# Kernel tuning notes

Hardware: AMD Instinct MI355X
Metric: run time of the kernel (lower is better)

## Reference

```python
import jax, jax.numpy as jnp
import numpy as np

M = 4096        # reference column size (init kwarg m)
TAU = 1.0       # temperature
SLICE_LEN = 4096


def setup_inputs() -> dict:
    key = jax.random.key(0)
    scores = jax.random.normal(key, (4, 131072), dtype=jnp.float32)
    return {"scores": scores}


def reference(scores):
    B, n = scores.shape
    m = min(M, n)
    # global top-m (sorted descending, matching torch.topk sorted=True)
    ref_val, ref_idx = jax.lax.top_k(scores, m)          # (B, m), (B, m)

    n_chunks = n // SLICE_LEN
    # (n_chunks, B, SLICE_LEN): scan over token chunks so only one
    # (B, SLICE_LEN, m) pairwise block is live at a time, as in the torch loop.
    chunks = jnp.swapaxes(scores.reshape(B, n_chunks, SLICE_LEN), 0, 1)

    def step(_, slice_scores):
        # pairwise = -|s_i - ref_j| / tau  -> softmax over m -> argmax -> gather
        pairwise = -jnp.abs(slice_scores[..., None] - ref_val[:, None, :]) / TAU
        P_hat = jax.nn.softmax(pairwise, axis=-1)        # (B, SLICE_LEN, m)
        col_rank = jnp.argmax(P_hat, axis=-1)            # (B, SLICE_LEN)
        perm_slice = jnp.take_along_axis(ref_idx, col_rank, axis=1)
        return None, perm_slice

    _, perms = jax.lax.scan(step, None, chunks)          # (n_chunks, B, SLICE_LEN)
    perm = jnp.swapaxes(perms, 0, 1).reshape(B, n)       # (B, n) int32 indices
    return perm
```

## Files before the change

### kernel.cpp

```cpp
#include <hip/hip_runtime.h>
#include <stdint.h>

#define BROWS 4
#define NCOLS 131072
#define MREF  4096
#define HIST_BITS 13
#define NBUCK (1 << HIST_BITS)
#define USHIFT (32 - HIST_BITS)
#define CAP 6144
#define HIST_BLK_PER_ROW 8
#define NPART 32
#define PQUOTA 192
#define PARTCAP 1024

__device__ __forceinline__ uint32_t orderable(float f) {
    uint32_t u = __float_as_uint(f);
    return (u & 0x80000000u) ? ~u : (u | 0x80000000u);
}
__device__ __forceinline__ float unorderable(uint32_t u) {
    uint32_t b = (u & 0x80000000u) ? (u & 0x7FFFFFFFu) : ~u;
    return __uint_as_float(b);
}

__global__ void k_zero(uint32_t* hist) {
    int i = blockIdx.x * blockDim.x + threadIdx.x;
    int tot = BROWS * NBUCK;
    for (; i < tot; i += gridDim.x * blockDim.x) hist[i] = 0u;
}

__global__ void k_hist(const float* __restrict__ sc, uint32_t* __restrict__ hist) {
    __shared__ uint32_t h[NBUCK];
    for (int t = threadIdx.x; t < NBUCK; t += blockDim.x) h[t] = 0u;
    __syncthreads();
    int row  = blockIdx.x / HIST_BLK_PER_ROW;
    int part = blockIdx.x % HIST_BLK_PER_ROW;
    const int CHUNK = NCOLS / HIST_BLK_PER_ROW;
    const float* p = sc + row * NCOLS + part * CHUNK;
    for (int c = threadIdx.x; c < CHUNK; c += blockDim.x) {
        uint32_t u = orderable(p[c]);
        atomicAdd(&h[u >> USHIFT], 1u);
    }
    __syncthreads();
    uint32_t* g = hist + (row << HIST_BITS);
    for (int t = threadIdx.x; t < NBUCK; t += blockDim.x) {
        uint32_t v = h[t];
        if (v) atomicAdd(&g[t], v);
    }
}

__global__ void k_thresh(const uint32_t* __restrict__ hist, uint32_t* __restrict__ Hrow,
                         int* __restrict__ Bs, uint32_t* __restrict__ pcur,
                         uint32_t* __restrict__ pse) {
    __shared__ uint32_t part[256];
    int row = blockIdx.x;
    const uint32_t* h = hist + (row << HIST_BITS);
    int bhi = NBUCK - 1 - (int)threadIdx.x * 32;
    uint32_t run = 0;
    for (int k = 0; k < 32; ++k) run += h[bhi - k];
    part[threadIdx.x] = run;
    __syncthreads();
    if (threadIdx.x == 0) {
        int      Bloc[NPART];
        uint32_t Ploc[NPART];
        for (int p = 0; p < NPART; ++p) { Bloc[p] = -1; Ploc[p] = 0u; }
        uint32_t cum = 0, T = 0;
        int H = 0, pi = 1;
        bool done = false;
        for (int t = 0; t < 256 && !done; ++t) {
            uint32_t cafter = cum + part[t];
            bool cross = (cafter >= (uint32_t)MREF) ||
                         (pi < NPART && cafter >= (uint32_t)(pi * PQUOTA));
            if (cross) {
                int tp = NBUCK - 1 - t * 32;
                for (int k2 = 0; k2 < 32 && !done; ++k2) {
                    int b = tp - k2;
                    uint32_t prev = cum;
                    cum += h[b];
                    while (pi < NPART && cum >= (uint32_t)(pi * PQUOTA)) {
                        Bloc[pi] = b; Ploc[pi] = prev; ++pi;
                    }
                    if (cum >= (uint32_t)MREF) { H = b; T = cum; done = true; }
                }
            } else {
                cum = cafter;
            }
        }
        for (int p = pi; p < NPART; ++p) { Bloc[p] = H - 1; Ploc[p] = T; }
        if (T > (uint32_t)CAP) T = (uint32_t)CAP;
        Hrow[row] = (uint32_t)H;
        Bs[row * NPART + 0] = NBUCK;
        for (int p = 1; p < NPART; ++p) Bs[row * NPART + p] = Bloc[p];
        for (int p = 0; p < NPART; ++p) {
            uint32_t st = Ploc[p];
            if (st > (uint32_t)CAP) st = (uint32_t)CAP;
            pcur[row * NPART + p] = st;
            pse[row * (NPART + 1) + p] = st;
        }
        pse[row * (NPART + 1) + NPART] = T;
    }
}

__global__ void k_compact(const float* __restrict__ sc, const uint32_t* __restrict__ Hrow,
                          const int* __restrict__ Bs, uint32_t* __restrict__ pcur,
                          uint64_t* __restrict__ cand) {
    __shared__ int bsL[NPART];
    __shared__ uint32_t cntP[NPART];
    __shared__ uint32_t baseP[NPART];
    int row = blockIdx.x >> 7;
    int base = (blockIdx.x & 127) << 10;
    uint32_t H = Hrow[row];
    if (threadIdx.x < NPART) {
        bsL[threadIdx.x] = Bs[row * NPART + threadIdx.x];
        cntP[threadIdx.x] = 0u;
    }
    __syncthreads();
    const float* p = sc + row * NCOLS + base;

    uint32_t myu[4], mycol[4], myr[4];
    int myp[4];
    uint32_t n = 0;
    for (int k = 0; k < 4; ++k) {
        int c = (int)threadIdx.x + (k << 8);
        uint32_t u = orderable(p[c]);
        uint32_t b = u >> USHIFT;
        if (b >= H) {
            int pp = 0;
            for (int q = 1; q < NPART; ++q) pp += ((int)b <= bsL[q]) ? 1 : 0;
            myu[n] = u; mycol[n] = (uint32_t)(base + c); myp[n] = pp;
            myr[n] = atomicAdd(&cntP[pp], 1u);
            ++n;
        }
    }
    __syncthreads();
    if (threadIdx.x < NPART)
        baseP[threadIdx.x] = atomicAdd(&pcur[row * NPART + threadIdx.x], cntP[threadIdx.x]);
    __syncthreads();
    uint64_t* cr = cand + (size_t)row * CAP;
    for (uint32_t k = 0; k < n; ++k) {
        uint32_t idx = baseP[myp[k]] + myr[k];
        if (idx < (uint32_t)CAP)
            cr[idx] = ((uint64_t)(~myu[k]) << 32) | mycol[k];
    }
}

__global__ void k_psort(const uint32_t* __restrict__ pse, uint64_t* __restrict__ cand,
                        float* __restrict__ rv, uint32_t* __restrict__ ri) {
    __shared__ uint64_t lds[PARTCAP];
    int row = blockIdx.x >> 5;
    int pp  = blockIdx.x & 31;
    uint32_t start = pse[row * (NPART + 1) + pp];
    uint32_t end   = pse[row * (NPART + 1) + pp + 1];
    if (end > (uint32_t)CAP) end = (uint32_t)CAP;
    uint32_t n = (end > start) ? (end - start) : 0u;
    if (n > (uint32_t)PARTCAP) n = (uint32_t)PARTCAP;
    uint64_t* seg = cand + (size_t)row * CAP + start;
    for (uint32_t i = threadIdx.x; i < (uint32_t)PARTCAP; i += blockDim.x)
        lds[i] = (i < n) ? seg[i] : ~0ULL;
    __syncthreads();
    for (uint32_t k = 2; k <= (uint32_t)PARTCAP; k <<= 1) {
        for (uint32_t j = k >> 1; j > 0; j >>= 1) {
            for (uint32_t i = threadIdx.x; i < (uint32_t)PARTCAP; i += blockDim.x) {
                uint32_t ixj = i ^ j;
                if (ixj > i) {
                    uint64_t a = lds[i], bb = lds[ixj];
                    bool up = ((i & k) == 0);
                    if ((a > bb) == up) { lds[i] = bb; lds[ixj] = a; }
                }
            }
            __syncthreads();
        }
    }
    for (uint32_t i = threadIdx.x; i < n; i += blockDim.x) {
        uint32_t gpos = start + i;
        if (gpos < (uint32_t)MREF) {
            uint64_t key = lds[i];
            uint32_t u = ~(uint32_t)(key >> 32);
            rv[row * MREF + gpos] = unorderable(u);
            ri[row * MREF + gpos] = (uint32_t)(key & 0xFFFFFFFFu);
        }
    }
}

__global__ void k_map(const float* __restrict__ sc, const float* __restrict__ rv,
                      const uint32_t* __restrict__ ri, int* __restrict__ out) {
    __shared__ float srv[MREF];
    int row = blockIdx.x >> 9;
    int col = ((blockIdx.x & 511) << 8) + threadIdx.x;
    const float* rvr = rv + row * MREF;
    for (int t = threadIdx.x; t < MREF; t += blockDim.x) srv[t] = rvr[t];
    __syncthreads();

    float s = sc[row * NCOLS + col];
    int lo = 0, hi = MREF;
    while (lo < hi) { int mid = (lo + hi) >> 1; if (srv[mid] <= s) hi = mid; else lo = mid + 1; }
    int p = lo, jmin;
    if (p == 0) jmin = 0;
    else if (p == MREF) jmin = MREF - 1;
    else {
        float dp = fabsf(s - srv[p]);
        float dm = fabsf(s - srv[p - 1]);
        jmin = (dm <= dp) ? (p - 1) : p;
    }
    float pmax = -fabsf(s - srv[jmin]);
    int jans = jmin;
    for (int j = jmin - 1; j >= 0; --j) {
        float pw = -fabsf(s - srv[j]);
        if (expf(pw - pmax) == 1.0f) jans = j; else break;
    }
    out[row * NCOLS + col] = (int)ri[row * MREF + jans];
}

extern "C" void kernel_launch(void* const* d_in, const int* in_sizes, int n_in,
                              void* d_out, int out_size, void* d_ws, size_t ws_size,
                              hipStream_t stream) {
    const float* sc = (const float*)d_in[0];
    int* out = (int*)d_out;
    char* w = (char*)d_ws;

    uint32_t* hist = (uint32_t*)w;
    uint32_t* Hrow = (uint32_t*)(w + 131072);
    int*      Bs   = (int*)     (w + 131200);
    uint32_t* pcur = (uint32_t*)(w + 131712);
    uint32_t* pse  = (uint32_t*)(w + 132224);
    uint64_t* cand = (uint64_t*)(w + 132864);
    float*    rv   = (float*)   (w + 329472);
    uint32_t* ri   = (uint32_t*)(w + 395008);

    k_zero   <<<64, 256, 0, stream>>>(hist);
    k_hist   <<<BROWS * HIST_BLK_PER_ROW, 256, 0, stream>>>(sc, hist);
    k_thresh <<<BROWS, 256, 0, stream>>>(hist, Hrow, Bs, pcur, pse);
    k_compact<<<512, 256, 0, stream>>>(sc, Hrow, Bs, pcur, cand);
    k_psort  <<<BROWS * NPART, 512, 0, stream>>>(pse, cand, rv, ri);
    k_map    <<<BROWS * 512, 256, 0, stream>>>(sc, rv, ri, out);
}
```

Before: 69.39 us.

## Drop zero and compact kernels; per-block histogram slots and fused partition scan in sort

Each histogram block now writes its private histogram to its own slot, and the threshold kernel sums the slots. This removes the zeroing kernel and the global atomics. The compaction kernel is removed: each partition-sort block scans the whole row and collects elements in its bucket range directly into LDS with a shared-memory atomic counter. This saves two launches and the candidate buffer round trip, but every one of the 128 sort blocks now reads a full 512KB row, so global read traffic grows about 32x for that stage.

Result: slower. 128.7 us (+85.4%).

```diff
diff --git a/kernel.cpp b/kernel.cpp
--- a/kernel.cpp
+++ b/kernel.cpp
@@ -7,7 +7,6 @@
 #define HIST_BITS 13
 #define NBUCK (1 << HIST_BITS)
 #define USHIFT (32 - HIST_BITS)
-#define CAP 6144
 #define HIST_BLK_PER_ROW 8
 #define NPART 32
 #define PQUOTA 192
@@ -22,13 +21,7 @@
     return __uint_as_float(b);
 }
 
-__global__ void k_zero(uint32_t* hist) {
-    int i = blockIdx.x * blockDim.x + threadIdx.x;
-    int tot = BROWS * NBUCK;
-    for (; i < tot; i += gridDim.x * blockDim.x) hist[i] = 0u;
-}
-
-__global__ void k_hist(const float* __restrict__ sc, uint32_t* __restrict__ hist) {
+__global__ void k_hist(const float* __restrict__ sc, uint32_t* __restrict__ hslot) {
     __shared__ uint32_t h[NBUCK];
     for (int t = threadIdx.x; t < NBUCK; t += blockDim.x) h[t] = 0u;
     __syncthreads();
@@ -41,19 +34,22 @@
         atomicAdd(&h[u >> USHIFT], 1u);
     }
     __syncthreads();
-    uint32_t* g = hist + (row << HIST_BITS);
-    for (int t = threadIdx.x; t < NBUCK; t += blockDim.x) {
-        uint32_t v = h[t];
-        if (v) atomicAdd(&g[t], v);
-    }
+    uint32_t* g = hslot + ((size_t)(row * HIST_BLK_PER_ROW + part)) * NBUCK;
+    for (int t = threadIdx.x; t < NBUCK; t += blockDim.x) g[t] = h[t];
 }
 
-__global__ void k_thresh(const uint32_t* __restrict__ hist, uint32_t* __restrict__ Hrow,
-                         int* __restrict__ Bs, uint32_t* __restrict__ pcur,
-                         uint32_t* __restrict__ pse) {
+__global__ void k_thresh(const uint32_t* __restrict__ hslot, uint32_t* __restrict__ Hrow,
+                         int* __restrict__ Bs, uint32_t* __restrict__ pse) {
+    __shared__ uint32_t h[NBUCK];
     __shared__ uint32_t part[256];
     int row = blockIdx.x;
-    const uint32_t* h = hist + (row << HIST_BITS);
+    const uint32_t* basep = hslot + (size_t)row * HIST_BLK_PER_ROW * NBUCK;
+    for (int t = threadIdx.x; t < NBUCK; t += blockDim.x) {
+        uint32_t s = 0;
+        for (int sl = 0; sl < HIST_BLK_PER_ROW; ++sl) s += basep[sl * NBUCK + t];
+        h[t] = s;
+    }
+    __syncthreads();
     int bhi = NBUCK - 1 - (int)threadIdx.x * 32;
     uint32_t run = 0;
     for (int k = 0; k < 32; ++k) run += h[bhi - k];
@@ -86,76 +82,42 @@
             }
         }
         for (int p = pi; p < NPART; ++p) { Bloc[p] = H - 1; Ploc[p] = T; }
-        if (T > (uint32_t)CAP) T = (uint32_t)CAP;
         Hrow[row] = (uint32_t)H;
-        Bs[row * NPART + 0] = NBUCK;
-        for (int p = 1; p < NPART; ++p) Bs[row * NPART + p] = Bloc[p];
-        for (int p = 0; p < NPART; ++p) {
-            uint32_t st = Ploc[p];
-            if (st > (uint32_t)CAP) st = (uint32_t)CAP;
-            pcur[row * NPART + p] = st;
-            pse[row * (NPART + 1) + p] = st;
-        }
+        Bs[row * (NPART + 1) + 0] = NBUCK;
+        for (int p = 1; p < NPART; ++p) Bs[row * (NPART + 1) + p] = Bloc[p];
+        Bs[row * (NPART + 1) + NPART] = H - 1;
+        for (int p = 0; p < NPART; ++p) pse[row * (NPART + 1) + p] = Ploc[p];
         pse[row * (NPART + 1) + NPART] = T;
     }
 }
 
-__global__ void k_compact(const float* __restrict__ sc, const uint32_t* __restrict__ Hrow,
-                          const int* __restrict__ Bs, uint32_t* __restrict__ pcur,
-                          uint64_t* __restrict__ cand) {
-    __shared__ int bsL[NPART];
-    __shared__ uint32_t cntP[NPART];
-    __shared__ uint32_t baseP[NPART];
-    int row = blockIdx.x >> 7;
-    int base = (blockIdx.x & 127) << 10;
-    uint32_t H = Hrow[row];
-    if (threadIdx.x < NPART) {
-        bsL[threadIdx.x] = Bs[row * NPART + threadIdx.x];
-        cntP[threadIdx.x] = 0u;
-    }
+__global__ void k_psort(const float* __restrict__ sc, const int* __restrict__ Bs,
+                        const uint32_t* __restrict__ pse,
+                        float* __restrict__ rv, uint32_t* __restrict__ ri) {
+    __shared__ uint64_t lds[PARTCAP];
+    __shared__ uint32_t cnt;
+    int row = blockIdx.x >> 5;
+    int pp  = blockIdx.x & 31;
+    int hi = Bs[row * (NPART + 1) + pp];
+    int lo = Bs[row * (NPART + 1) + pp + 1];
+    uint32_t start = pse[row * (NPART + 1) + pp];
+    if (threadIdx.x == 0) cnt = 0u;
     __syncthreads();
-    const float* p = sc + row * NCOLS + base;
-
-    uint32_t myu[4], mycol[4], myr[4];
-    int myp[4];
-    uint32_t n = 0;
-    for (int k = 0; k < 4; ++k) {
-        int c = (int)threadIdx.x + (k << 8);
+    const float* p = sc + row * NCOLS;
+    for (int c = (int)threadIdx.x; c < NCOLS; c += (int)blockDim.x) {
         uint32_t u = orderable(p[c]);
-        uint32_t b = u >> USHIFT;
-        if (b >= H) {
-            int pp = 0;
-            for (int q = 1; q < NPART; ++q) pp += ((int)b <= bsL[q]) ? 1 : 0;
-            myu[n] = u; mycol[n] = (uint32_t)(base + c); myp[n] = pp;
-            myr[n] = atomicAdd(&cntP[pp], 1u);
-            ++n;
+        int b = (int)(u >> USHIFT);
+        if (b > lo && b <= hi) {
+            uint32_t pos = atomicAdd(&cnt, 1u);
+            if (pos < (uint32_t)PARTCAP)
+                lds[pos] = ((uint64_t)(~u) << 32) | (uint32_t)c;
         }
     }
     __syncthreads();
-    if (threadIdx.x < NPART)
-        baseP[threadIdx.x] = atomicAdd(&pcur[row * NPART + threadIdx.x], cntP[threadIdx.x]);
-    __syncthreads();
-    uint64_t* cr = cand + (size_t)row * CAP;
-    for (uint32_t k = 0; k < n; ++k) {
-        uint32_t idx = baseP[myp[k]] + myr[k];
-        if (idx < (uint32_t)CAP)
-            cr[idx] = ((uint64_t)(~myu[k]) << 32) | mycol[k];
-    }
-}
-
-__global__ void k_psort(const uint32_t* __restrict__ pse, uint64_t* __restrict__ cand,
-                        float* __restrict__ rv, uint32_t* __restrict__ ri) {
-    __shared__ uint64_t lds[PARTCAP];
-    int row = blockIdx.x >> 5;
-    int pp  = blockIdx.x & 31;
-    uint32_t start = pse[row * (NPART + 1) + pp];
-    uint32_t end   = pse[row * (NPART + 1) + pp + 1];
-    if (end > (uint32_t)CAP) end = (uint32_t)CAP;
-    uint32_t n = (end > start) ? (end - start) : 0u;
+    uint32_t n = cnt;
     if (n > (uint32_t)PARTCAP) n = (uint32_t)PARTCAP;
-    uint64_t* seg = cand + (size_t)row * CAP + start;
-    for (uint32_t i = threadIdx.x; i < (uint32_t)PARTCAP; i += blockDim.x)
-        lds[i] = (i < n) ? seg[i] : ~0ULL;
+    for (uint32_t i = n + threadIdx.x; i < (uint32_t)PARTCAP; i += blockDim.x)
+        lds[i] = ~0ULL;
     __syncthreads();
     for (uint32_t k = 2; k <= (uint32_t)PARTCAP; k <<= 1) {
         for (uint32_t j = k >> 1; j > 0; j >>= 1) {
@@ -217,19 +179,15 @@
     int* out = (int*)d_out;
     char* w = (char*)d_ws;
 
-    uint32_t* hist = (uint32_t*)w;
-    uint32_t* Hrow = (uint32_t*)(w + 131072);
-    int*      Bs   = (int*)     (w + 131200);
-    uint32_t* pcur = (uint32_t*)(w + 131712);
-    uint32_t* pse  = (uint32_t*)(w + 132224);
-    uint64_t* cand = (uint64_t*)(w + 132864);
-    float*    rv   = (float*)   (w + 329472);
-    uint32_t* ri   = (uint32_t*)(w + 395008);
+    uint32_t* hslot = (uint32_t*)w;
+    uint32_t* Hrow  = (uint32_t*)(w + 1048576);
+    int*      Bs    = (int*)     (w + 1048704);
+    uint32_t* pse   = (uint32_t*)(w + 1049344);
+    float*    rv    = (float*)   (w + 1049984);
+    uint32_t* ri    = (uint32_t*)(w + 1115520);
 
-    k_zero   <<<64, 256, 0, stream>>>(hist);
-    k_hist   <<<BROWS * HIST_BLK_PER_ROW, 256, 0, stream>>>(sc, hist);
-    k_thresh <<<BROWS, 256, 0, stream>>>(hist, Hrow, Bs, pcur, pse);
-    k_compact<<<512, 256, 0, stream>>>(sc, Hrow, Bs, pcur, cand);
-    k_psort  <<<BROWS * NPART, 512, 0, stream>>>(pse, cand, rv, ri);
+    k_hist   <<<BROWS * HIST_BLK_PER_ROW, 256, 0, stream>>>(sc, hslot);
+    k_thresh <<<BROWS, 256, 0, stream>>>(hslot, Hrow, Bs, pse);
+    k_psort  <<<BROWS * NPART, 512, 0, stream>>>(sc, Bs, pse, rv, ri);
     k_map    <<<BROWS * 512, 256, 0, stream>>>(sc, rv, ri, out);
 }
```
